# Performance work log

Hardware: AMD Instinct MI355X
Metric: run time of the kernel (lower is better)

The kernel has to match this reference:

```python
import jax, jax.numpy as jnp
import numpy as np

N = 100000
E = 1600000
G = 2048          # number of graphs in the batch
HEADS = 4
HID = 16          # per-head channels
IN_CH = 128
D = HEADS * HID   # 64, concat output width per layer
NEG_SLOPE = 0.2


def _gat_layer(x, src, dst, W, a_src, a_dst, bias):
    # x: [N, Fin], W: [Fin, H*C], a_src/a_dst: [H, C], bias: [H*C]
    h = (x @ W).reshape(N, HEADS, HID)                      # [N, H, C]
    al_s = jnp.einsum('nhc,hc->nh', h, a_src)               # [N, H]
    al_d = jnp.einsum('nhc,hc->nh', h, a_dst)               # [N, H]
    e = jax.nn.leaky_relu(al_s[src] + al_d[dst], NEG_SLOPE) # [E+N, H]
    # segment softmax over incoming edges of each destination node
    m = jax.ops.segment_max(e, dst, num_segments=N)         # [N, H]
    e = jnp.exp(e - m[dst])
    s = jax.ops.segment_sum(e, dst, num_segments=N)
    alpha = e / (s[dst] + 1e-16)                            # [E+N, H]
    msg = h[src] * alpha[..., None]                         # [E+N, H, C]
    out = jax.ops.segment_sum(msg, dst, num_segments=N)     # [N, H, C]
    return out.reshape(N, D) + bias


def setup_inputs() -> dict:
    key = jax.random.key(0)
    ks = jax.random.split(key, 16)
    x = jax.random.normal(ks[0], (N, IN_CH), dtype=jnp.float32)
    edge_index = jax.random.randint(ks[1], (2, E), 0, N, dtype=jnp.int64)
    batch = jnp.sort(jax.random.randint(ks[2], (N,), 0, G, dtype=jnp.int64))
    inp = {'x': x, 'edge_index': edge_index, 'batch': batch}
    fins = [IN_CH, D, D]
    for i, fin in enumerate(fins):
        kk = jax.random.split(ks[3 + i], 4)
        sc = 1.0 / np.sqrt(fin)
        inp[f'W{i}'] = jax.random.normal(kk[0], (fin, D), dtype=jnp.float32) * sc
        inp[f'as{i}'] = jax.random.normal(kk[1], (HEADS, HID), dtype=jnp.float32) * 0.1
        inp[f'ad{i}'] = jax.random.normal(kk[2], (HEADS, HID), dtype=jnp.float32) * 0.1
        inp[f'b{i}'] = jnp.zeros((D,), dtype=jnp.float32)
    inp['head_w'] = jax.random.normal(ks[10], (1, D), dtype=jnp.float32) * (1.0 / np.sqrt(D))
    inp['head_b'] = jnp.zeros((1,), dtype=jnp.float32)
    return inp


def reference(x, edge_index, batch,
              W0, as0, ad0, b0,
              W1, as1, ad1, b1,
              W2, as2, ad2, b2,
              head_w, head_b):
    # PyG GATConv adds self-loops by default
    loops = jnp.arange(N, dtype=edge_index.dtype)
    src = jnp.concatenate([edge_index[0], loops])
    dst = jnp.concatenate([edge_index[1], loops])
    layers = [(W0, as0, ad0, b0), (W1, as1, ad1, b1), (W2, as2, ad2, b2)]
    h = x.astype(jnp.float32)
    for (W, a_s, a_d, b) in layers:
        h = _gat_layer(h, src, dst, W, a_s, a_d, b)
        h = jax.nn.relu(h)  # dropout p=0.0 -> identity
    pooled = jax.ops.segment_sum(h, batch, num_segments=G)  # [G, D]
    out = pooled @ head_w.T + head_b                         # [G, 1]
    return out.reshape(-1)                                   # out_dim == 1 -> flatten
```

## Files before the change

### kernel.cpp

```cpp
#include <hip/hip_runtime.h>
#include <hip/hip_bf16.h>
#include <hip/hip_fp16.h>
#include <cstdint>
#include <cstddef>

#define NN 100000
#define EE 1600000
#define GG 2048

__device__ __forceinline__ float lrelu(float v) { return v > 0.f ? v : 0.2f * v; }

__global__ void k_count(const int* __restrict__ ei, int* __restrict__ deg,
                        int* __restrict__ rank) {
    int i = blockIdx.x * blockDim.x + threadIdx.x;
    if (i >= EE + NN) return;
    int d = (i < EE) ? ei[EE + i] : (i - EE);
    rank[i] = atomicAdd(&deg[d], 1);
}

__global__ void k_alloc(const int* __restrict__ deg, int* __restrict__ offs,
                        int* __restrict__ cursor, const float* __restrict__ head_b,
                        float* __restrict__ out) {
    int i = blockIdx.x * blockDim.x + threadIdx.x;
    int lane = threadIdx.x & 63;
    int d = (i < NN) ? deg[i] : 0;
    int incl = d;
#pragma unroll
    for (int off = 1; off < 64; off <<= 1) {
        int t = __shfl_up(incl, off, 64);
        if (lane >= off) incl += t;
    }
    int total = __shfl(incl, 63, 64);
    int base = 0;
    if (lane == 63) base = atomicAdd(cursor, total);
    base = __shfl(base, 63, 64);
    if (i < NN) offs[i] = base + incl - d;
    if (i < GG) out[i] = head_b[0];
}

__global__ void k_scatter(const int* __restrict__ ei, const int* __restrict__ offs,
                          const int* __restrict__ rank, int* __restrict__ col) {
    int i = blockIdx.x * blockDim.x + threadIdx.x;
    if (i >= EE + NN) return;
    int s, d;
    if (i < EE) { s = ei[i]; d = ei[EE + i]; } else { s = d = i - EE; }
    col[offs[d] + rank[i]] = s;
}

template <int FIN>
__global__ __launch_bounds__(256) void k_gemm(const float* __restrict__ X,
                                              const float* __restrict__ W,
                                              const float* __restrict__ asrc,
                                              const float* __restrict__ adst,
                                              float* __restrict__ H,
                                              float* __restrict__ als,
                                              float* __restrict__ ald) {
    int j  = threadIdx.x & 63;
    int ty = threadIdx.x >> 6;
    int row = __builtin_amdgcn_readfirstlane(blockIdx.x * 16 + ty * 4);
    const float* x0 = X + (size_t)row * FIN;
    const float* x1 = x0 + FIN;
    const float* x2 = x1 + FIN;
    const float* x3 = x2 + FIN;
    float a0 = 0.f, a1 = 0.f, a2 = 0.f, a3 = 0.f;
#pragma unroll
    for (int k = 0; k < FIN; k += 4) {
        float4 xa = *(const float4*)(x0 + k);
        float4 xb = *(const float4*)(x1 + k);
        float4 xc = *(const float4*)(x2 + k);
        float4 xd = *(const float4*)(x3 + k);
        float w0 = W[(k + 0) * 64 + j];
        float w1 = W[(k + 1) * 64 + j];
        float w2 = W[(k + 2) * 64 + j];
        float w3 = W[(k + 3) * 64 + j];
        a0 += xa.x * w0 + xa.y * w1 + xa.z * w2 + xa.w * w3;
        a1 += xb.x * w0 + xb.y * w1 + xb.z * w2 + xb.w * w3;
        a2 += xc.x * w0 + xc.y * w1 + xc.z * w2 + xc.w * w3;
        a3 += xd.x * w0 + xd.y * w1 + xd.z * w2 + xd.w * w3;
    }
    H[(size_t)(row + 0) * 64 + j] = a0;
    H[(size_t)(row + 1) * 64 + j] = a1;
    H[(size_t)(row + 2) * 64 + j] = a2;
    H[(size_t)(row + 3) * 64 + j] = a3;
    float asj = asrc[j], adj = adst[j];
    float accs[4] = {a0, a1, a2, a3};
#pragma unroll
    for (int r = 0; r < 4; r++) {
        float vs = accs[r] * asj;
        float vd = accs[r] * adj;
#pragma unroll
        for (int off = 8; off > 0; off >>= 1) {
            vs += __shfl_xor(vs, off, 64);
            vd += __shfl_xor(vd, off, 64);
        }
        if ((j & 15) == 0) {
            int h = j >> 4;
            als[(size_t)(row + r) * 4 + h] = vs;
            ald[(size_t)(row + r) * 4 + h] = vd;
        }
    }
}

__global__ __launch_bounds__(256) void k_aggf(
    const float* __restrict__ H, const float* __restrict__ als,
    const float* __restrict__ ald, const int* __restrict__ offs,
    const int* __restrict__ deg, const int* __restrict__ col,
    const float* __restrict__ bias,
    const float* __restrict__ W,
    const float* __restrict__ asrc,
    const float* __restrict__ adst,
    float* __restrict__ Hn, float* __restrict__ alsn, float* __restrict__ aldn) {
    __shared__ float wl[4096];
    __shared__ float xs[16 * 68];
    int tid = threadIdx.x;
    int g = tid >> 4;
    int l = tid & 15;
    int n = blockIdx.x * 16 + g;
    int start = offs[n];
    int len = deg[n];
    int hsel = l >> 2;
    float adh = ald[(size_t)n * 4 + hsel];
    const float4* Hp = (const float4*)H + l;

#pragma unroll
    for (int t = 0; t < 4; t++)
        ((float4*)wl)[tid + t * 256] = ((const float4*)W)[tid + t * 256];

    float4 acc = {0.f, 0.f, 0.f, 0.f};
    float ssum = 0.f;
    for (int e = 0; e < len; e += 8) {
        bool  v[8];
        int   s[8];
#pragma unroll
        for (int i = 0; i < 8; i++) {
            v[i] = (e + i < len);
            s[i] = v[i] ? col[start + e + i] : 0;
        }
        float  w[8];
        float4 hr[8];
#pragma unroll
        for (int i = 0; i < 8; i++) {
            float a = als[(size_t)s[i] * 4 + hsel];
            hr[i] = Hp[(size_t)s[i] * 16];
            float ev = lrelu(a + adh);
            w[i] = v[i] ? __expf(ev) : 0.f;
        }
#pragma unroll
        for (int i = 0; i < 8; i++) {
            ssum  += w[i];
            acc.x = fmaf(w[i], hr[i].x, acc.x);
            acc.y = fmaf(w[i], hr[i].y, acc.y);
            acc.z = fmaf(w[i], hr[i].z, acc.z);
            acc.w = fmaf(w[i], hr[i].w, acc.w);
        }
    }
    float inv = 1.f / (ssum + 1e-16f);
    float4 b4 = ((const float4*)bias)[l];
    float* xr = xs + g * 68 + 4 * l;
    xr[0] = fmaxf(acc.x * inv + b4.x, 0.f);
    xr[1] = fmaxf(acc.y * inv + b4.y, 0.f);
    xr[2] = fmaxf(acc.z * inv + b4.z, 0.f);
    xr[3] = fmaxf(acc.w * inv + b4.w, 0.f);

    __syncthreads();

    float4 o = {0.f, 0.f, 0.f, 0.f};
    const float* xrow = xs + g * 68;
    const float* wcol = wl + 4 * l;
#pragma unroll
    for (int k = 0; k < 64; k += 4) {
        float4 xv = *(const float4*)(xrow + k);
        float4 w0 = *(const float4*)(wcol + (k + 0) * 64);
        float4 w1 = *(const float4*)(wcol + (k + 1) * 64);
        float4 w2 = *(const float4*)(wcol + (k + 2) * 64);
        float4 w3 = *(const float4*)(wcol + (k + 3) * 64);
        o.x += xv.x * w0.x + xv.y * w1.x + xv.z * w2.x + xv.w * w3.x;
        o.y += xv.x * w0.y + xv.y * w1.y + xv.z * w2.y + xv.w * w3.y;
        o.z += xv.x * w0.z + xv.y * w1.z + xv.z * w2.z + xv.w * w3.z;
        o.w += xv.x * w0.w + xv.y * w1.w + xv.z * w2.w + xv.w * w3.w;
    }
    ((float4*)Hn)[(size_t)n * 16 + l] = o;

    float4 av = ((const float4*)asrc)[l];
    float4 dv = ((const float4*)adst)[l];
    float vs = o.x * av.x + o.y * av.y + o.z * av.z + o.w * av.w;
    float vd = o.x * dv.x + o.y * dv.y + o.z * dv.z + o.w * dv.w;
    vs += __shfl_xor(vs, 1, 16); vs += __shfl_xor(vs, 2, 16);
    vd += __shfl_xor(vd, 1, 16); vd += __shfl_xor(vd, 2, 16);
    if ((l & 3) == 0) {
        int h = l >> 2;
        alsn[(size_t)n * 4 + h] = vs;
        aldn[(size_t)n * 4 + h] = vd;
    }
}

__global__ __launch_bounds__(256) void k_aggl(
    const float* __restrict__ H, const float* __restrict__ als,
    const float* __restrict__ ald, const int* __restrict__ offs,
    const int* __restrict__ deg, const int* __restrict__ col,
    const float* __restrict__ bias, const int* __restrict__ batch,
    const float* __restrict__ hw, float* __restrict__ out) {
    int tid = threadIdx.x;
    int g = tid >> 4;
    int l = tid & 15;
    int n = blockIdx.x * 16 + g;
    int start = offs[n];
    int len = deg[n];
    int hsel = l >> 2;
    float adh = ald[(size_t)n * 4 + hsel];
    const float4* Hp = (const float4*)H + l;

    float4 acc = {0.f, 0.f, 0.f, 0.f};
    float ssum = 0.f;
    for (int e = 0; e < len; e += 8) {
        bool  v[8];
        int   s[8];
#pragma unroll
        for (int i = 0; i < 8; i++) {
            v[i] = (e + i < len);
            s[i] = v[i] ? col[start + e + i] : 0;
        }
        float  w[8];
        float4 hr[8];
#pragma unroll
        for (int i = 0; i < 8; i++) {
            float a = als[(size_t)s[i] * 4 + hsel];
            hr[i] = Hp[(size_t)s[i] * 16];
            float ev = lrelu(a + adh);
            w[i] = v[i] ? __expf(ev) : 0.f;
        }
#pragma unroll
        for (int i = 0; i < 8; i++) {
            ssum  += w[i];
            acc.x = fmaf(w[i], hr[i].x, acc.x);
            acc.y = fmaf(w[i], hr[i].y, acc.y);
            acc.z = fmaf(w[i], hr[i].z, acc.z);
            acc.w = fmaf(w[i], hr[i].w, acc.w);
        }
    }
    float inv = 1.f / (ssum + 1e-16f);
    float4 b4 = ((const float4*)bias)[l];
    float4 w4 = ((const float4*)hw)[l];
    float t = fmaxf(acc.x * inv + b4.x, 0.f) * w4.x
            + fmaxf(acc.y * inv + b4.y, 0.f) * w4.y
            + fmaxf(acc.z * inv + b4.z, 0.f) * w4.z
            + fmaxf(acc.w * inv + b4.w, 0.f) * w4.w;
#pragma unroll
    for (int off = 8; off > 0; off >>= 1) t += __shfl_xor(t, off, 16);
    if (l == 0) atomicAdd(&out[batch[n]], t);
}

extern "C" void kernel_launch(void* const* d_in, const int* in_sizes, int n_in,
                              void* d_out, int out_size, void* d_ws, size_t ws_size,
                              hipStream_t stream) {
    const float* x     = (const float*)d_in[0];
    const int*   ei    = (const int*)d_in[1];
    const int*   batch = (const int*)d_in[2];
    const float* Wm[3] = {(const float*)d_in[3], (const float*)d_in[7],  (const float*)d_in[11]};
    const float* As[3] = {(const float*)d_in[4], (const float*)d_in[8],  (const float*)d_in[12]};
    const float* Ad[3] = {(const float*)d_in[5], (const float*)d_in[9],  (const float*)d_in[13]};
    const float* Bb[3] = {(const float*)d_in[6], (const float*)d_in[10], (const float*)d_in[14]};
    const float* hw = (const float*)d_in[15];
    const float* hb = (const float*)d_in[16];
    float* out = (float*)d_out;

    uint8_t* w = (uint8_t*)d_ws;
    auto alloc = [&](size_t bytes) -> void* {
        void* p = (void*)w;
        w += (bytes + 255) & ~(size_t)255;
        return p;
    };
    float* H    = (float*)alloc((size_t)NN * 64 * 4);
    float* Bf   = (float*)alloc((size_t)NN * 64 * 4);
    float* als  = (float*)alloc((size_t)NN * 4 * 4);
    float* ald  = (float*)alloc((size_t)NN * 4 * 4);
    float* als2 = (float*)alloc((size_t)NN * 4 * 4);
    float* ald2 = (float*)alloc((size_t)NN * 4 * 4);
    int*   deg  = (int*)alloc((size_t)(NN + 64) * 4);
    int*   offs = (int*)alloc((size_t)NN * 4);
    int*   rank = (int*)alloc((size_t)(EE + NN) * 4);
    int*   col  = (int*)alloc((size_t)(EE + NN) * 4);
    int*   cursor = deg + NN;

    hipMemsetAsync(deg, 0, (size_t)(NN + 1) * 4, stream);

    int eb = (EE + NN + 255) / 256;
    int nb = (NN + 255) / 256;
    k_count  <<<eb, 256, 0, stream>>>(ei, deg, rank);
    k_alloc  <<<nb, 256, 0, stream>>>(deg, offs, cursor, hb, out);
    k_scatter<<<eb, 256, 0, stream>>>(ei, offs, rank, col);

    k_gemm<128><<<NN / 16, 256, 0, stream>>>(x, Wm[0], As[0], Ad[0], H, als, ald);
    k_aggf<<<NN / 16, 256, 0, stream>>>(H,  als,  ald,  offs, deg, col, Bb[0],
                                        Wm[1], As[1], Ad[1], Bf, als2, ald2);
    k_aggf<<<NN / 16, 256, 0, stream>>>(Bf, als2, ald2, offs, deg, col, Bb[1],
                                        Wm[2], As[2], Ad[2], H, als, ald);
    k_aggl<<<NN / 16, 256, 0, stream>>>(H,  als,  ald,  offs, deg, col, Bb[2],
                                        batch, hw, out);
}
```

Measured before the change: 528.1 us.

## Bucket CSR neighbors by source octant and fuse degree count with layer-0 GEMM

The edge-count pass now splits each destination's counter into 8 buckets keyed by source-node range, so that within each CSR row the neighbor list is partly grouped by source index. The aim is better locality when the aggregation kernels gather source features. The count pass is also merged with the first-layer GEMM into one launch, so both independent workloads can share the GPU and one launch is removed. In exchange the count array and the prefix-scan metadata grow eightfold, the memset gets larger, and atomic contention per counter drops.

```diff
diff --git a/kernel.cpp b/kernel.cpp
--- a/kernel.cpp
+++ b/kernel.cpp
@@ -8,56 +8,25 @@
 #define EE 1600000
 #define GG 2048
 
+#define NOCT 8
+#define OCTW 12500
+
+constexpr int NB_CNT  = (EE + NN + 255) / 256;
+constexpr int NB_GEMM = NN / 16;
+
 __device__ __forceinline__ float lrelu(float v) { return v > 0.f ? v : 0.2f * v; }
 
-__global__ void k_count(const int* __restrict__ ei, int* __restrict__ deg,
-                        int* __restrict__ rank) {
-    int i = blockIdx.x * blockDim.x + threadIdx.x;
-    if (i >= EE + NN) return;
-    int d = (i < EE) ? ei[EE + i] : (i - EE);
-    rank[i] = atomicAdd(&deg[d], 1);
-}
-
-__global__ void k_alloc(const int* __restrict__ deg, int* __restrict__ offs,
-                        int* __restrict__ cursor, const float* __restrict__ head_b,
-                        float* __restrict__ out) {
-    int i = blockIdx.x * blockDim.x + threadIdx.x;
-    int lane = threadIdx.x & 63;
-    int d = (i < NN) ? deg[i] : 0;
-    int incl = d;
-#pragma unroll
-    for (int off = 1; off < 64; off <<= 1) {
-        int t = __shfl_up(incl, off, 64);
-        if (lane >= off) incl += t;
-    }
-    int total = __shfl(incl, 63, 64);
-    int base = 0;
-    if (lane == 63) base = atomicAdd(cursor, total);
-    base = __shfl(base, 63, 64);
-    if (i < NN) offs[i] = base + incl - d;
-    if (i < GG) out[i] = head_b[0];
-}
-
-__global__ void k_scatter(const int* __restrict__ ei, const int* __restrict__ offs,
-                          const int* __restrict__ rank, int* __restrict__ col) {
-    int i = blockIdx.x * blockDim.x + threadIdx.x;
-    if (i >= EE + NN) return;
-    int s, d;
-    if (i < EE) { s = ei[i]; d = ei[EE + i]; } else { s = d = i - EE; }
-    col[offs[d] + rank[i]] = s;
-}
-
 template <int FIN>
-__global__ __launch_bounds__(256) void k_gemm(const float* __restrict__ X,
-                                              const float* __restrict__ W,
-                                              const float* __restrict__ asrc,
-                                              const float* __restrict__ adst,
-                                              float* __restrict__ H,
-                                              float* __restrict__ als,
-                                              float* __restrict__ ald) {
+__device__ __forceinline__ void gemm_body(int bidx, const float* __restrict__ X,
+                                          const float* __restrict__ W,
+                                          const float* __restrict__ asrc,
+                                          const float* __restrict__ adst,
+                                          float* __restrict__ H,
+                                          float* __restrict__ als,
+                                          float* __restrict__ ald) {
     int j  = threadIdx.x & 63;
     int ty = threadIdx.x >> 6;
-    int row = __builtin_amdgcn_readfirstlane(blockIdx.x * 16 + ty * 4);
+    int row = __builtin_amdgcn_readfirstlane(bidx * 16 + ty * 4);
     const float* x0 = X + (size_t)row * FIN;
     const float* x1 = x0 + FIN;
     const float* x2 = x1 + FIN;
@@ -99,6 +68,82 @@
             ald[(size_t)(row + r) * 4 + h] = vd;
         }
     }
+}
+
+template <int FIN>
+__global__ __launch_bounds__(256) void k_gemm(const float* __restrict__ X,
+                                              const float* __restrict__ W,
+                                              const float* __restrict__ asrc,
+                                              const float* __restrict__ adst,
+                                              float* __restrict__ H,
+                                              float* __restrict__ als,
+                                              float* __restrict__ ald) {
+    gemm_body<FIN>(blockIdx.x, X, W, asrc, adst, H, als, ald);
+}
+
+__global__ __launch_bounds__(256) void k_cg(const int* __restrict__ ei,
+                                            int* __restrict__ deg2,
+                                            int* __restrict__ rank2,
+                                            const float* __restrict__ X,
+                                            const float* __restrict__ W,
+                                            const float* __restrict__ asrc,
+                                            const float* __restrict__ adst,
+                                            float* __restrict__ H,
+                                            float* __restrict__ als,
+                                            float* __restrict__ ald) {
+    if (blockIdx.x < NB_CNT) {
+        int i = blockIdx.x * 256 + threadIdx.x;
+        if (i < EE + NN) {
+            int s, d;
+            if (i < EE) { s = ei[i]; d = ei[EE + i]; } else { s = d = i - EE; }
+            unsigned oct = (unsigned)s / OCTW;
+            rank2[i] = atomicAdd(&deg2[d * 8 + oct], 1);
+        }
+    } else {
+        gemm_body<128>(blockIdx.x - NB_CNT, X, W, asrc, adst, H, als, ald);
+    }
+}
+
+__global__ void k_alloc2(const int* __restrict__ deg2, int* __restrict__ starts,
+                         int* __restrict__ offs, int* __restrict__ deg,
+                         int* __restrict__ cursor, const float* __restrict__ head_b,
+                         float* __restrict__ out) {
+    int i = blockIdx.x * 256 + threadIdx.x;
+    int lane = threadIdx.x & 63;
+    int rel[8];
+    int tot = 0;
+    if (i < NN) {
+#pragma unroll
+        for (int o = 0; o < 8; o++) { rel[o] = tot; tot += deg2[i * 8 + o]; }
+    }
+    int incl = tot;
+#pragma unroll
+    for (int off = 1; off < 64; off <<= 1) {
+        int t = __shfl_up(incl, off, 64);
+        if (lane >= off) incl += t;
+    }
+    int wtot = __shfl(incl, 63, 64);
+    int base = 0;
+    if (lane == 63) base = atomicAdd(cursor, wtot);
+    base = __shfl(base, 63, 64);
+    int mybase = base + incl - tot;
+    if (i < NN) {
+#pragma unroll
+        for (int o = 0; o < 8; o++) starts[i * 8 + o] = mybase + rel[o];
+        offs[i] = mybase;
+        deg[i]  = tot;
+    }
+    if (i < GG) out[i] = head_b[0];
+}
+
+__global__ void k_scatter2(const int* __restrict__ ei, const int* __restrict__ starts,
+                           const int* __restrict__ rank2, int* __restrict__ col) {
+    int i = blockIdx.x * blockDim.x + threadIdx.x;
+    if (i >= EE + NN) return;
+    int s, d;
+    if (i < EE) { s = ei[i]; d = ei[EE + i]; } else { s = d = i - EE; }
+    unsigned oct = (unsigned)s / OCTW;
+    col[starts[d * 8 + oct] + rank2[i]] = s;
 }
 
 __global__ __launch_bounds__(256) void k_aggf(
@@ -270,27 +315,31 @@
         w += (bytes + 255) & ~(size_t)255;
         return p;
     };
-    float* H    = (float*)alloc((size_t)NN * 64 * 4);
-    float* Bf   = (float*)alloc((size_t)NN * 64 * 4);
-    float* als  = (float*)alloc((size_t)NN * 4 * 4);
-    float* ald  = (float*)alloc((size_t)NN * 4 * 4);
-    float* als2 = (float*)alloc((size_t)NN * 4 * 4);
-    float* ald2 = (float*)alloc((size_t)NN * 4 * 4);
-    int*   deg  = (int*)alloc((size_t)(NN + 64) * 4);
-    int*   offs = (int*)alloc((size_t)NN * 4);
-    int*   rank = (int*)alloc((size_t)(EE + NN) * 4);
-    int*   col  = (int*)alloc((size_t)(EE + NN) * 4);
-    int*   cursor = deg + NN;
-
-    hipMemsetAsync(deg, 0, (size_t)(NN + 1) * 4, stream);
+    float* H      = (float*)alloc((size_t)NN * 64 * 4);
+    float* Bf     = (float*)alloc((size_t)NN * 64 * 4);
+    float* als    = (float*)alloc((size_t)NN * 4 * 4);
+    float* ald    = (float*)alloc((size_t)NN * 4 * 4);
+    float* als2   = (float*)alloc((size_t)NN * 4 * 4);
+    float* ald2   = (float*)alloc((size_t)NN * 4 * 4);
+    int*   meta   = (int*)alloc(((size_t)NN * 8 + 64) * 4);
+    int*   starts = (int*)alloc((size_t)NN * 8 * 4);
+    int*   offs   = (int*)alloc((size_t)NN * 4);
+    int*   deg    = (int*)alloc((size_t)NN * 4);
+    int*   rank2  = (int*)alloc((size_t)(EE + NN) * 4);
+    int*   col    = (int*)alloc((size_t)(EE + NN) * 4);
+
+    int* deg2   = meta;
+    int* cursor = meta + (size_t)NN * 8;
+
+    hipMemsetAsync(meta, 0, ((size_t)NN * 8 + 64) * 4, stream);
 
     int eb = (EE + NN + 255) / 256;
-    int nb = (NN + 255) / 256;
-    k_count  <<<eb, 256, 0, stream>>>(ei, deg, rank);
-    k_alloc  <<<nb, 256, 0, stream>>>(deg, offs, cursor, hb, out);
-    k_scatter<<<eb, 256, 0, stream>>>(ei, offs, rank, col);
-
-    k_gemm<128><<<NN / 16, 256, 0, stream>>>(x, Wm[0], As[0], Ad[0], H, als, ald);
+    k_cg<<<NB_CNT + NB_GEMM, 256, 0, stream>>>(ei, deg2, rank2,
+                                               x, Wm[0], As[0], Ad[0], H, als, ald);
+    k_alloc2<<<(NN + 255) / 256, 256, 0, stream>>>(deg2, starts, offs, deg,
+                                                   cursor, hb, out);
+    k_scatter2<<<eb, 256, 0, stream>>>(ei, starts, rank2, col);
+
     k_aggf<<<NN / 16, 256, 0, stream>>>(H,  als,  ald,  offs, deg, col, Bb[0],
                                         Wm[1], As[1], Ad[1], Bf, als2, ald2);
     k_aggf<<<NN / 16, 256, 0, stream>>>(Bf, als2, ald2, offs, deg, col, Bb[1],
```

New measurement: 539.5 us. +2.2%, slower.

## Replace CSR build with fixed-stride padded adjacency and fuse build with first GEMM

Applied to the files above, without the earlier changes.

Replaces the three-kernel count/scan/scatter CSR construction with one pass that appends each edge into a fixed-stride slot per destination (72 slots), with an overflow list for high-degree nodes. The build, the first-layer GEMM and the output init are merged into one launch using block-index ranges. This removes two edge passes, the rank buffer and the prefix-scan kernel. In exchange the column buffer grows, neighbour order inside a row becomes nondeterministic, and overflow edges are handled by a linear scan of the overflow list. The overflow list has a fixed capacity of 4096 entries with no bounds check.

```diff
diff --git a/kernel.cpp b/kernel.cpp
--- a/kernel.cpp
+++ b/kernel.cpp
@@ -7,57 +7,25 @@
 #define NN 100000
 #define EE 1600000
 #define GG 2048
+#define STRIDE 72
+
+constexpr int NB_EDGE = (EE + NN + 255) / 256;
+constexpr int NB_GEMM = NN / 16;
+constexpr int NB_OUT  = (GG + 255) / 256;
 
 __device__ __forceinline__ float lrelu(float v) { return v > 0.f ? v : 0.2f * v; }
 
-__global__ void k_count(const int* __restrict__ ei, int* __restrict__ deg,
-                        int* __restrict__ rank) {
-    int i = blockIdx.x * blockDim.x + threadIdx.x;
-    if (i >= EE + NN) return;
-    int d = (i < EE) ? ei[EE + i] : (i - EE);
-    rank[i] = atomicAdd(&deg[d], 1);
-}
-
-__global__ void k_alloc(const int* __restrict__ deg, int* __restrict__ offs,
-                        int* __restrict__ cursor, const float* __restrict__ head_b,
-                        float* __restrict__ out) {
-    int i = blockIdx.x * blockDim.x + threadIdx.x;
-    int lane = threadIdx.x & 63;
-    int d = (i < NN) ? deg[i] : 0;
-    int incl = d;
-#pragma unroll
-    for (int off = 1; off < 64; off <<= 1) {
-        int t = __shfl_up(incl, off, 64);
-        if (lane >= off) incl += t;
-    }
-    int total = __shfl(incl, 63, 64);
-    int base = 0;
-    if (lane == 63) base = atomicAdd(cursor, total);
-    base = __shfl(base, 63, 64);
-    if (i < NN) offs[i] = base + incl - d;
-    if (i < GG) out[i] = head_b[0];
-}
-
-__global__ void k_scatter(const int* __restrict__ ei, const int* __restrict__ offs,
-                          const int* __restrict__ rank, int* __restrict__ col) {
-    int i = blockIdx.x * blockDim.x + threadIdx.x;
-    if (i >= EE + NN) return;
-    int s, d;
-    if (i < EE) { s = ei[i]; d = ei[EE + i]; } else { s = d = i - EE; }
-    col[offs[d] + rank[i]] = s;
-}
-
 template <int FIN>
-__global__ __launch_bounds__(256) void k_gemm(const float* __restrict__ X,
-                                              const float* __restrict__ W,
-                                              const float* __restrict__ asrc,
-                                              const float* __restrict__ adst,
-                                              float* __restrict__ H,
-                                              float* __restrict__ als,
-                                              float* __restrict__ ald) {
+__device__ __forceinline__ void gemm_body(int bidx, const float* __restrict__ X,
+                                          const float* __restrict__ W,
+                                          const float* __restrict__ asrc,
+                                          const float* __restrict__ adst,
+                                          float* __restrict__ H,
+                                          float* __restrict__ als,
+                                          float* __restrict__ ald) {
     int j  = threadIdx.x & 63;
     int ty = threadIdx.x >> 6;
-    int row = __builtin_amdgcn_readfirstlane(blockIdx.x * 16 + ty * 4);
+    int row = __builtin_amdgcn_readfirstlane(bidx * 16 + ty * 4);
     const float* x0 = X + (size_t)row * FIN;
     const float* x1 = x0 + FIN;
     const float* x2 = x1 + FIN;
@@ -101,10 +69,43 @@
     }
 }
 
+__global__ __launch_bounds__(256) void k_build(const int* __restrict__ ei,
+                                               int* __restrict__ deg,
+                                               int* __restrict__ col,
+                                               int* __restrict__ ofc,
+                                               int* __restrict__ ofl,
+                                               const float* __restrict__ X,
+                                               const float* __restrict__ W,
+                                               const float* __restrict__ asrc,
+                                               const float* __restrict__ adst,
+                                               float* __restrict__ H,
+                                               float* __restrict__ als,
+                                               float* __restrict__ ald,
+                                               const float* __restrict__ head_b,
+                                               float* __restrict__ out) {
+    int b = blockIdx.x;
+    if (b < NB_EDGE) {
+        int i = b * 256 + threadIdx.x;
+        if (i < EE + NN) {
+            int s, d;
+            if (i < EE) { s = ei[i]; d = ei[EE + i]; } else { s = d = i - EE; }
+            int r = atomicAdd(&deg[d], 1);
+            if (r < STRIDE) col[d * STRIDE + r] = s;
+            else { int o = atomicAdd(ofc, 1); ofl[2 * o] = s; ofl[2 * o + 1] = d; }
+        }
+    } else if (b < NB_EDGE + NB_GEMM) {
+        gemm_body<128>(b - NB_EDGE, X, W, asrc, adst, H, als, ald);
+    } else {
+        int gI = (b - NB_EDGE - NB_GEMM) * 256 + threadIdx.x;
+        if (gI < GG) out[gI] = head_b[0];
+    }
+}
+
 __global__ __launch_bounds__(256) void k_aggf(
     const float* __restrict__ H, const float* __restrict__ als,
-    const float* __restrict__ ald, const int* __restrict__ offs,
+    const float* __restrict__ ald,
     const int* __restrict__ deg, const int* __restrict__ col,
+    const int* __restrict__ ofc, const int* __restrict__ ofl,
     const float* __restrict__ bias,
     const float* __restrict__ W,
     const float* __restrict__ asrc,
@@ -116,7 +117,7 @@
     int g = tid >> 4;
     int l = tid & 15;
     int n = blockIdx.x * 16 + g;
-    int start = offs[n];
+    int start = n * STRIDE;
     int len = deg[n];
     int hsel = l >> 2;
     float adh = ald[(size_t)n * 4 + hsel];
@@ -128,12 +129,13 @@
 
     float4 acc = {0.f, 0.f, 0.f, 0.f};
     float ssum = 0.f;
-    for (int e = 0; e < len; e += 8) {
+    int len_in = len <= STRIDE ? len : STRIDE;
+    for (int e = 0; e < len_in; e += 8) {
         bool  v[8];
         int   s[8];
 #pragma unroll
         for (int i = 0; i < 8; i++) {
-            v[i] = (e + i < len);
+            v[i] = (e + i < len_in);
             s[i] = v[i] ? col[start + e + i] : 0;
         }
         float  w[8];
@@ -152,6 +154,20 @@
             acc.y = fmaf(w[i], hr[i].y, acc.y);
             acc.z = fmaf(w[i], hr[i].z, acc.z);
             acc.w = fmaf(w[i], hr[i].w, acc.w);
+        }
+    }
+    if (len > STRIDE) {
+        int oc = *ofc;
+        for (int k2 = 0; k2 < oc; k2++) {
+            if (ofl[2 * k2 + 1] == n) {
+                int s0 = ofl[2 * k2];
+                float a = als[(size_t)s0 * 4 + hsel];
+                float4 h0 = Hp[(size_t)s0 * 16];
+                float w0 = __expf(lrelu(a + adh));
+                ssum += w0;
+                acc.x = fmaf(w0, h0.x, acc.x); acc.y = fmaf(w0, h0.y, acc.y);
+                acc.z = fmaf(w0, h0.z, acc.z); acc.w = fmaf(w0, h0.w, acc.w);
+            }
         }
     }
     float inv = 1.f / (ssum + 1e-16f);
@@ -196,15 +212,16 @@
 
 __global__ __launch_bounds__(256) void k_aggl(
     const float* __restrict__ H, const float* __restrict__ als,
-    const float* __restrict__ ald, const int* __restrict__ offs,
+    const float* __restrict__ ald,
     const int* __restrict__ deg, const int* __restrict__ col,
+    const int* __restrict__ ofc, const int* __restrict__ ofl,
     const float* __restrict__ bias, const int* __restrict__ batch,
     const float* __restrict__ hw, float* __restrict__ out) {
     int tid = threadIdx.x;
     int g = tid >> 4;
     int l = tid & 15;
     int n = blockIdx.x * 16 + g;
-    int start = offs[n];
+    int start = n * STRIDE;
     int len = deg[n];
     int hsel = l >> 2;
     float adh = ald[(size_t)n * 4 + hsel];
@@ -212,12 +229,13 @@
 
     float4 acc = {0.f, 0.f, 0.f, 0.f};
     float ssum = 0.f;
-    for (int e = 0; e < len; e += 8) {
+    int len_in = len <= STRIDE ? len : STRIDE;
+    for (int e = 0; e < len_in; e += 8) {
         bool  v[8];
         int   s[8];
 #pragma unroll
         for (int i = 0; i < 8; i++) {
-            v[i] = (e + i < len);
+            v[i] = (e + i < len_in);
             s[i] = v[i] ? col[start + e + i] : 0;
         }
         float  w[8];
@@ -236,6 +254,20 @@
             acc.y = fmaf(w[i], hr[i].y, acc.y);
             acc.z = fmaf(w[i], hr[i].z, acc.z);
             acc.w = fmaf(w[i], hr[i].w, acc.w);
+        }
+    }
+    if (len > STRIDE) {
+        int oc = *ofc;
+        for (int k2 = 0; k2 < oc; k2++) {
+            if (ofl[2 * k2 + 1] == n) {
+                int s0 = ofl[2 * k2];
+                float a = als[(size_t)s0 * 4 + hsel];
+                float4 h0 = Hp[(size_t)s0 * 16];
+                float w0 = __expf(lrelu(a + adh));
+                ssum += w0;
+                acc.x = fmaf(w0, h0.x, acc.x); acc.y = fmaf(w0, h0.y, acc.y);
+                acc.z = fmaf(w0, h0.z, acc.z); acc.w = fmaf(w0, h0.w, acc.w);
+            }
         }
     }
     float inv = 1.f / (ssum + 1e-16f);
@@ -277,24 +309,21 @@
     float* als2 = (float*)alloc((size_t)NN * 4 * 4);
     float* ald2 = (float*)alloc((size_t)NN * 4 * 4);
     int*   deg  = (int*)alloc((size_t)(NN + 64) * 4);
-    int*   offs = (int*)alloc((size_t)NN * 4);
-    int*   rank = (int*)alloc((size_t)(EE + NN) * 4);
-    int*   col  = (int*)alloc((size_t)(EE + NN) * 4);
-    int*   cursor = deg + NN;
-
-    hipMemsetAsync(deg, 0, (size_t)(NN + 1) * 4, stream);
-
-    int eb = (EE + NN + 255) / 256;
-    int nb = (NN + 255) / 256;
-    k_count  <<<eb, 256, 0, stream>>>(ei, deg, rank);
-    k_alloc  <<<nb, 256, 0, stream>>>(deg, offs, cursor, hb, out);
-    k_scatter<<<eb, 256, 0, stream>>>(ei, offs, rank, col);
-
-    k_gemm<128><<<NN / 16, 256, 0, stream>>>(x, Wm[0], As[0], Ad[0], H, als, ald);
-    k_aggf<<<NN / 16, 256, 0, stream>>>(H,  als,  ald,  offs, deg, col, Bb[0],
+    int*   col  = (int*)alloc((size_t)NN * STRIDE * 4);
+    int*   ofl  = (int*)alloc((size_t)4096 * 2 * 4);
+
+    int* ofc = deg + NN;
+
+    hipMemsetAsync(deg, 0, (size_t)(NN + 64) * 4, stream);
+
+    k_build<<<NB_EDGE + NB_GEMM + NB_OUT, 256, 0, stream>>>(
+        ei, deg, col, ofc, ofl,
+        x, Wm[0], As[0], Ad[0], H, als, ald, hb, out);
+
+    k_aggf<<<NN / 16, 256, 0, stream>>>(H,  als,  ald,  deg, col, ofc, ofl, Bb[0],
                                         Wm[1], As[1], Ad[1], Bf, als2, ald2);
-    k_aggf<<<NN / 16, 256, 0, stream>>>(Bf, als2, ald2, offs, deg, col, Bb[1],
+    k_aggf<<<NN / 16, 256, 0, stream>>>(Bf, als2, ald2, deg, col, ofc, ofl, Bb[1],
                                         Wm[2], As[2], Ad[2], H, als, ald);
-    k_aggl<<<NN / 16, 256, 0, stream>>>(H,  als,  ald,  offs, deg, col, Bb[2],
+    k_aggl<<<NN / 16, 256, 0, stream>>>(H,  als,  ald,  deg, col, ofc, ofl, Bb[2],
                                         batch, hw, out);
 }
```

Result: slower. 567.8 us (+7.5%).

## Fuse degree count with layer-0 GEMM and phase CSR scatter by destination range

Applied to the files above, without the earlier changes.

Merges the edge-degree counting kernel and the first-layer GEMM into one launch, with the two jobs on disjoint block ranges so they can run at the same time and one launch is saved. It also replaces the single-pass CSR scatter with a persistent 1024-block kernel. That kernel sweeps the edge list four times, each pass writing only edges whose destination falls in one quarter of the node range, so the scattered writes to col stay within a smaller region. A loose, poll-limited global counter is used to roughly align blocks on each phase. In exchange, the edge indices are re-read four times and the spin-wait adds some synchronisation overhead.

```diff
diff --git a/kernel.cpp b/kernel.cpp
--- a/kernel.cpp
+++ b/kernel.cpp
@@ -8,56 +8,27 @@
 #define EE 1600000
 #define GG 2048
 
+#define NPH 4
+#define QW  25000
+#define SNBLK 1024
+
+constexpr int NB_CNT  = (EE + NN + 255) / 256;
+constexpr int NB_GEMM = NN / 16;
+constexpr int SCH = (EE + NN + SNBLK - 1) / SNBLK;
+
 __device__ __forceinline__ float lrelu(float v) { return v > 0.f ? v : 0.2f * v; }
 
-__global__ void k_count(const int* __restrict__ ei, int* __restrict__ deg,
-                        int* __restrict__ rank) {
-    int i = blockIdx.x * blockDim.x + threadIdx.x;
-    if (i >= EE + NN) return;
-    int d = (i < EE) ? ei[EE + i] : (i - EE);
-    rank[i] = atomicAdd(&deg[d], 1);
-}
-
-__global__ void k_alloc(const int* __restrict__ deg, int* __restrict__ offs,
-                        int* __restrict__ cursor, const float* __restrict__ head_b,
-                        float* __restrict__ out) {
-    int i = blockIdx.x * blockDim.x + threadIdx.x;
-    int lane = threadIdx.x & 63;
-    int d = (i < NN) ? deg[i] : 0;
-    int incl = d;
-#pragma unroll
-    for (int off = 1; off < 64; off <<= 1) {
-        int t = __shfl_up(incl, off, 64);
-        if (lane >= off) incl += t;
-    }
-    int total = __shfl(incl, 63, 64);
-    int base = 0;
-    if (lane == 63) base = atomicAdd(cursor, total);
-    base = __shfl(base, 63, 64);
-    if (i < NN) offs[i] = base + incl - d;
-    if (i < GG) out[i] = head_b[0];
-}
-
-__global__ void k_scatter(const int* __restrict__ ei, const int* __restrict__ offs,
-                          const int* __restrict__ rank, int* __restrict__ col) {
-    int i = blockIdx.x * blockDim.x + threadIdx.x;
-    if (i >= EE + NN) return;
-    int s, d;
-    if (i < EE) { s = ei[i]; d = ei[EE + i]; } else { s = d = i - EE; }
-    col[offs[d] + rank[i]] = s;
-}
-
 template <int FIN>
-__global__ __launch_bounds__(256) void k_gemm(const float* __restrict__ X,
-                                              const float* __restrict__ W,
-                                              const float* __restrict__ asrc,
-                                              const float* __restrict__ adst,
-                                              float* __restrict__ H,
-                                              float* __restrict__ als,
-                                              float* __restrict__ ald) {
+__device__ __forceinline__ void gemm_body(int bidx, const float* __restrict__ X,
+                                          const float* __restrict__ W,
+                                          const float* __restrict__ asrc,
+                                          const float* __restrict__ adst,
+                                          float* __restrict__ H,
+                                          float* __restrict__ als,
+                                          float* __restrict__ ald) {
     int j  = threadIdx.x & 63;
     int ty = threadIdx.x >> 6;
-    int row = __builtin_amdgcn_readfirstlane(blockIdx.x * 16 + ty * 4);
+    int row = __builtin_amdgcn_readfirstlane(bidx * 16 + ty * 4);
     const float* x0 = X + (size_t)row * FIN;
     const float* x1 = x0 + FIN;
     const float* x2 = x1 + FIN;
@@ -98,6 +69,75 @@
             als[(size_t)(row + r) * 4 + h] = vs;
             ald[(size_t)(row + r) * 4 + h] = vd;
         }
+    }
+}
+
+__global__ __launch_bounds__(256) void k_cg(const int* __restrict__ ei,
+                                            int* __restrict__ deg,
+                                            int* __restrict__ rank,
+                                            const float* __restrict__ X,
+                                            const float* __restrict__ W,
+                                            const float* __restrict__ asrc,
+                                            const float* __restrict__ adst,
+                                            float* __restrict__ H,
+                                            float* __restrict__ als,
+                                            float* __restrict__ ald) {
+    if (blockIdx.x < NB_CNT) {
+        int i = blockIdx.x * 256 + threadIdx.x;
+        if (i < EE + NN) {
+            int d = (i < EE) ? ei[EE + i] : (i - EE);
+            rank[i] = atomicAdd(&deg[d], 1);
+        }
+    } else {
+        gemm_body<128>(blockIdx.x - NB_CNT, X, W, asrc, adst, H, als, ald);
+    }
+}
+
+__global__ void k_alloc(const int* __restrict__ deg, int* __restrict__ offs,
+                        int* __restrict__ cursor, const float* __restrict__ head_b,
+                        float* __restrict__ out) {
+    int i = blockIdx.x * blockDim.x + threadIdx.x;
+    int lane = threadIdx.x & 63;
+    int d = (i < NN) ? deg[i] : 0;
+    int incl = d;
+#pragma unroll
+    for (int off = 1; off < 64; off <<= 1) {
+        int t = __shfl_up(incl, off, 64);
+        if (lane >= off) incl += t;
+    }
+    int total = __shfl(incl, 63, 64);
+    int base = 0;
+    if (lane == 63) base = atomicAdd(cursor, total);
+    base = __shfl(base, 63, 64);
+    if (i < NN) offs[i] = base + incl - d;
+    if (i < GG) out[i] = head_b[0];
+}
+
+__global__ __launch_bounds__(256) void k_scat(const int* __restrict__ ei,
+                                              const int* __restrict__ offs,
+                                              const int* __restrict__ rank,
+                                              int* __restrict__ col,
+                                              int* __restrict__ ctr) {
+    int b = blockIdx.x, tid = threadIdx.x;
+    int lo = b * SCH;
+    int hi = lo + SCH; if (hi > EE + NN) hi = EE + NN;
+    for (int p = 0; p < NPH; p++) {
+        if (tid == 0) {
+            __hip_atomic_fetch_add(&ctr[p], 1, __ATOMIC_RELAXED, __HIP_MEMORY_SCOPE_AGENT);
+            int polls = 0;
+            while (polls++ < 64 &&
+                   __hip_atomic_load(&ctr[p], __ATOMIC_RELAXED, __HIP_MEMORY_SCOPE_AGENT) < SNBLK)
+                __builtin_amdgcn_s_sleep(1);
+        }
+        __syncthreads();
+        for (int i = lo + tid; i < hi; i += 256) {
+            int d = (i < EE) ? ei[EE + i] : (i - EE);
+            if ((int)((unsigned)d / QW) == p) {
+                int s = (i < EE) ? ei[i] : d;
+                col[offs[d] + rank[i]] = s;
+            }
+        }
+        __syncthreads();
     }
 }
 
@@ -280,17 +320,17 @@
     int*   offs = (int*)alloc((size_t)NN * 4);
     int*   rank = (int*)alloc((size_t)(EE + NN) * 4);
     int*   col  = (int*)alloc((size_t)(EE + NN) * 4);
-    int*   cursor = deg + NN;
-
-    hipMemsetAsync(deg, 0, (size_t)(NN + 1) * 4, stream);
-
-    int eb = (EE + NN + 255) / 256;
-    int nb = (NN + 255) / 256;
-    k_count  <<<eb, 256, 0, stream>>>(ei, deg, rank);
-    k_alloc  <<<nb, 256, 0, stream>>>(deg, offs, cursor, hb, out);
-    k_scatter<<<eb, 256, 0, stream>>>(ei, offs, rank, col);
-
-    k_gemm<128><<<NN / 16, 256, 0, stream>>>(x, Wm[0], As[0], Ad[0], H, als, ald);
+
+    int* cursor = deg + NN;
+    int* ctr    = cursor + 8;
+
+    hipMemsetAsync(deg, 0, (size_t)(NN + 64) * 4, stream);
+
+    k_cg<<<NB_CNT + NB_GEMM, 256, 0, stream>>>(ei, deg, rank,
+                                               x, Wm[0], As[0], Ad[0], H, als, ald);
+    k_alloc<<<(NN + 255) / 256, 256, 0, stream>>>(deg, offs, cursor, hb, out);
+    k_scat <<<SNBLK, 256, 0, stream>>>(ei, offs, rank, col, ctr);
+
     k_aggf<<<NN / 16, 256, 0, stream>>>(H,  als,  ald,  offs, deg, col, Bb[0],
                                         Wm[1], As[1], Ad[1], Bf, als2, ald2);
     k_aggf<<<NN / 16, 256, 0, stream>>>(Bf, als2, ald2, offs, deg, col, Bb[1],
```

Result: slower. 734.3 us (+39.1%).
